# Optimization experiments

Hardware: AMD Instinct MI355X
Metric: run time of the kernel (lower is better)

The kernel has to match this reference:

```python
import jax, jax.numpy as jnp
import numpy as np

# Geometry constants (from init_kwargs)
LO = jnp.array([-51.2, -51.2, -3.0], dtype=jnp.float32)
HI = jnp.array([51.2, 51.2, 3.0], dtype=jnp.float32)
VS = jnp.array([0.2, 0.2, 6.0], dtype=jnp.float32)
NY, NX = 512, 512
BN_EPS = 1e-3  # mmdet3d BN1d default eps


def setup_inputs() -> dict:
    key = jax.random.key(0)
    ks = jax.random.split(key, 11)
    # points uniform inside point_cloud_range -> no points dropped by voxelizer
    points = jax.random.uniform(ks[0], (2, 120000, 3), dtype=jnp.float32) * (HI - LO) + LO
    C2, C = 32, 64
    w0 = jax.random.normal(ks[1], (8, C2), dtype=jnp.float32) / np.sqrt(8.0)
    g0 = jax.random.uniform(ks[2], (C2,), jnp.float32, 0.5, 1.5)
    b0 = jax.random.normal(ks[3], (C2,), jnp.float32) * 0.1
    m0 = jax.random.normal(ks[4], (C2,), jnp.float32) * 0.1
    v0 = jax.random.uniform(ks[5], (C2,), jnp.float32, 0.5, 1.5)
    w1 = jax.random.normal(ks[6], (C, C), dtype=jnp.float32) / np.sqrt(float(C))
    g1 = jax.random.uniform(ks[7], (C,), jnp.float32, 0.5, 1.5)
    b1 = jax.random.normal(ks[8], (C,), jnp.float32) * 0.1
    m1 = jax.random.normal(ks[9], (C,), jnp.float32) * 0.1
    v1 = jax.random.uniform(ks[10], (C,), jnp.float32, 0.5, 1.5)
    return dict(points=points, w0=w0, g0=g0, b0=b0, m0=m0, v0=v0,
                w1=w1, g1=g1, b1=b1, m1=m1, v1=v1)


def _bn(x, g, b, m, v):
    return (x - m) * jax.lax.rsqrt(v + BN_EPS) * g + b


def _embed_one(pts, w0, g0, b0, m0, v0, w1, g1, b1, m1, v1):
    # pts: [N, 3]. Dynamic voxelization: pillar index per point.
    xi = jnp.clip(jnp.floor((pts[:, 0] - LO[0]) / VS[0]).astype(jnp.int32), 0, NX - 1)
    yi = jnp.clip(jnp.floor((pts[:, 1] - LO[1]) / VS[1]).astype(jnp.int32), 0, NY - 1)
    vid = yi * NX + xi                       # flat pillar id, [N]
    nseg = NY * NX
    cnt = jax.ops.segment_sum(jnp.ones_like(pts[:, 0]), vid, nseg)  # [nseg]
    # cluster center offsets (mean xyz per pillar)
    mean = jax.ops.segment_sum(pts, vid, nseg) / jnp.maximum(cnt, 1.0)[:, None]
    f_cluster = pts - mean[vid]              # [N, 3]
    # pillar center offsets (x, y)
    cx = (xi.astype(pts.dtype) + 0.5) * VS[0] + LO[0]
    cy = (yi.astype(pts.dtype) + 0.5) * VS[1] + LO[1]
    f_center = jnp.stack([pts[:, 0] - cx, pts[:, 1] - cy], axis=-1)  # [N, 2]
    feats = jnp.concatenate([pts, f_cluster, f_center], axis=-1)     # [N, 8]
    # PFN layer 0: Linear(no bias) -> BN -> ReLU, then scatter-max + concat back
    h = jax.nn.relu(_bn(feats @ w0, g0, b0, m0, v0))                 # [N, 32]
    pooled0 = jax.ops.segment_max(h, vid, nseg)
    pooled0 = jnp.where(cnt[:, None] > 0, pooled0, 0.0)
    h = jnp.concatenate([h, pooled0[vid]], axis=-1)                  # [N, 64]
    # PFN layer 1 (last): per-point features, then scatter-max -> voxel feats
    h = jax.nn.relu(_bn(h @ w1, g1, b1, m1, v1))                     # [N, 64]
    vox = jax.ops.segment_max(h, vid, nseg)
    vox = jnp.where(cnt[:, None] > 0, vox, 0.0)                      # [nseg, 64]
    # PointPillarsScatter: dense BEV canvas [C, NY, NX]
    canvas = vox.reshape(NY, NX, -1).transpose(2, 0, 1)
    return canvas, h


def reference(points, w0, g0, b0, m0, v0, w1, g1, b1, m1, v1):
    canvases, point_feats = jax.vmap(
        lambda p: _embed_one(p, w0, g0, b0, m0, v0, w1, g1, b1, m1, v1)
    )(points)
    # canvases: [B, C, NY, NX] (torch.cat of per-sample pseudoimages over dim 0)
    return canvases, point_feats
```

## Files before the change

kernel.cpp:

```cpp
#include <hip/hip_runtime.h>

#define NPT   120000
#define NB    2
#define NSEG  262144
#define NXg   512
#define NSEGT (NB * NSEG)
#define NPTS  (NB * NPT)

typedef __attribute__((ext_vector_type(8))) short  bf16x8;
typedef __attribute__((ext_vector_type(4))) float  f32x4;

__device__ __forceinline__ unsigned short f2bf(float f) {
    unsigned u = __float_as_uint(f);
    return (unsigned short)((u + 0x7FFFu + ((u >> 16) & 1u)) >> 16);
}

__global__ __launch_bounds__(256) void k_init(unsigned int* __restrict__ cnt,
                                              const float* __restrict__ w1,
                                              const float* __restrict__ g1,
                                              const float* __restrict__ b1,
                                              const float* __restrict__ m1,
                                              const float* __restrict__ v1,
                                              unsigned short* __restrict__ wtbf,
                                              float* __restrict__ bias1f) {
    int t = threadIdx.x;
    if (blockIdx.x < 512) {
        int idx = blockIdx.x * 256 + t;
        ((uint4*)cnt)[idx] = make_uint4(0u, 0u, 0u, 0u);
        return;
    }
    #pragma unroll
    for (int i = 0; i < 16; ++i) {
        int idx = t + i * 256;
        int c = idx >> 6, k = idx & 63;
        float al = g1[c] * rsqrtf(v1[c] + 1e-3f);
        wtbf[idx] = f2bf(w1[k * 64 + c] * al);
    }
    if (t < 64) bias1f[t] = b1[t] - m1[t] * (g1[t] * rsqrtf(v1[t] + 1e-3f));
}

__global__ __launch_bounds__(256) void k_stats(const float* __restrict__ pts,
                                               unsigned int* __restrict__ cnt,
                                               unsigned int* __restrict__ rank) {
    int tid = blockIdx.x * 256 + threadIdx.x;
    if (tid >= NPTS) return;
    const float* p = pts + (size_t)tid * 3;
    float x = p[0], y = p[1];
    int xi = (int)floorf((x - (-51.2f)) / 0.2f);
    int yi = (int)floorf((y - (-51.2f)) / 0.2f);
    xi = min(max(xi, 0), 511);
    yi = min(max(yi, 0), 511);
    int b = (tid >= NPT) ? 1 : 0;
    int gvid = b * NSEG + (yi * NXg + xi);
    rank[tid] = atomicAdd(&cnt[gvid], 1u);
}

__global__ __launch_bounds__(256) void k_scan1(const unsigned int* __restrict__ cnt,
                                               unsigned int* __restrict__ offs,
                                               unsigned int* __restrict__ bsum) {
    __shared__ unsigned int s[256];
    int t = threadIdx.x;
    size_t base = (size_t)blockIdx.x * 1024 + t * 4;
    uint4 c4 = *(const uint4*)(cnt + base);
    unsigned int tsum = c4.x + c4.y + c4.z + c4.w;
    s[t] = tsum;
    __syncthreads();
    for (int o = 1; o < 256; o <<= 1) {
        unsigned int v = (t >= o) ? s[t - o] : 0u;
        __syncthreads();
        s[t] += v;
        __syncthreads();
    }
    unsigned int pre = s[t] - tsum;
    if (t == 255) bsum[blockIdx.x] = s[255];
    uint4 o4;
    o4.x = pre; o4.y = pre + c4.x; o4.z = o4.y + c4.y; o4.w = o4.z + c4.z;
    *(uint4*)(offs + base) = o4;
}

__global__ __launch_bounds__(256) void k_scan2(unsigned int* __restrict__ bsum) {
    __shared__ unsigned int s[256];
    int t = threadIdx.x;
    unsigned int a = bsum[2 * t], b = bsum[2 * t + 1];
    unsigned int ts = a + b;
    s[t] = ts;
    __syncthreads();
    for (int o = 1; o < 256; o <<= 1) {
        unsigned int v = (t >= o) ? s[t - o] : 0u;
        __syncthreads();
        s[t] += v;
        __syncthreads();
    }
    unsigned int pre = s[t] - ts;
    bsum[2 * t] = pre;
    bsum[2 * t + 1] = pre + a;
}

__global__ __launch_bounds__(256) void k_reorder(const float* __restrict__ pts,
                                                 const unsigned int* __restrict__ rank,
                                                 const unsigned int* __restrict__ offs,
                                                 const unsigned int* __restrict__ bsum,
                                                 float4* __restrict__ sxyz,
                                                 unsigned int* __restrict__ comb) {
    int tid = blockIdx.x * 256 + threadIdx.x;
    if (tid >= NPTS) return;
    const float* p = pts + (size_t)tid * 3;
    float x = p[0], y = p[1], z = p[2];
    int xi = (int)floorf((x - (-51.2f)) / 0.2f);
    int yi = (int)floorf((y - (-51.2f)) / 0.2f);
    xi = min(max(xi, 0), 511);
    yi = min(max(yi, 0), 511);
    int b = (tid >= NPT) ? 1 : 0;
    int gvid = b * NSEG + (yi * NXg + xi);
    unsigned pos = offs[gvid] + bsum[gvid >> 10] + rank[tid];
    sxyz[pos] = make_float4(x, y, z, __int_as_float(gvid));
    comb[pos] = ((unsigned)(gvid & 63) << 18) | (unsigned)tid;
}

__global__ __launch_bounds__(256) void k_pfn0(const float4* __restrict__ sxyz,
                                              const unsigned int* __restrict__ offs,
                                              const unsigned int* __restrict__ bsum,
                                              const unsigned int* __restrict__ cnt,
                                              const float* __restrict__ w0,
                                              const float* __restrict__ g0,
                                              const float* __restrict__ b0,
                                              const float* __restrict__ m0,
                                              const float* __restrict__ v0,
                                              unsigned short* __restrict__ xbf) {
    __shared__ float w0f[256];
    __shared__ float bias0[32];
    int t = threadIdx.x;
    {
        int c = t & 31;
        float al = g0[c] * rsqrtf(v0[c] + 1e-3f);
        w0f[t] = w0[t] * al;
        if (t < 32) bias0[t] = b0[t] - m0[t] * al;
    }
    __syncthreads();

    int pos = blockIdx.x * 256 + t;
    if (pos >= NPTS) return;

    float4 me = sxyz[pos];
    int gvid = __float_as_int(me.w);
    int vid = gvid & (NSEG - 1);
    int xi = vid & (NXg - 1), yi = vid >> 9;

    unsigned off = offs[gvid] + bsum[gvid >> 10];
    unsigned n   = cnt[gvid];
    float sx = 0.f, sy = 0.f, sz = 0.f;
    for (unsigned i = 0; i < n; ++i) {
        float4 q = sxyz[off + i];
        sx += q.x; sy += q.y; sz += q.z;
    }
    float inv = 1.0f / (float)n;
    float mx = sx * inv, my = sy * inv, mz = sz * inv;
    float cx = ((float)xi + 0.5f) * 0.2f + (-51.2f);
    float cy = ((float)yi + 0.5f) * 0.2f + (-51.2f);

    float own[32], pool[32];
    #pragma unroll
    for (int c = 0; c < 32; ++c) { pool[c] = 0.0f; own[c] = 0.0f; }
    for (unsigned i = 0; i < n; ++i) {
        float4 q = sxyz[off + i];
        float f[8] = {q.x, q.y, q.z, q.x - mx, q.y - my, q.z - mz,
                      q.x - cx, q.y - cy};
        bool self = (off + i == (unsigned)pos);
        #pragma unroll
        for (int c = 0; c < 32; ++c) {
            float acc = bias0[c];
            #pragma unroll
            for (int k = 0; k < 8; ++k) acc += f[k] * w0f[k * 32 + c];
            acc = fmaxf(acc, 0.0f);
            pool[c] = fmaxf(pool[c], acc);
            if (self) own[c] = acc;
        }
    }

    unsigned wv[16];
    uint4* dst = (uint4*)(xbf + (size_t)pos * 64);
    #pragma unroll
    for (int c2 = 0; c2 < 16; ++c2)
        wv[c2] = (unsigned)f2bf(own[2 * c2]) | ((unsigned)f2bf(own[2 * c2 + 1]) << 16);
    dst[0] = make_uint4(wv[0],  wv[1],  wv[2],  wv[3]);
    dst[1] = make_uint4(wv[4],  wv[5],  wv[6],  wv[7]);
    dst[2] = make_uint4(wv[8],  wv[9],  wv[10], wv[11]);
    dst[3] = make_uint4(wv[12], wv[13], wv[14], wv[15]);
    #pragma unroll
    for (int c2 = 0; c2 < 16; ++c2)
        wv[c2] = (unsigned)f2bf(pool[2 * c2]) | ((unsigned)f2bf(pool[2 * c2 + 1]) << 16);
    dst[4] = make_uint4(wv[0],  wv[1],  wv[2],  wv[3]);
    dst[5] = make_uint4(wv[4],  wv[5],  wv[6],  wv[7]);
    dst[6] = make_uint4(wv[8],  wv[9],  wv[10], wv[11]);
    dst[7] = make_uint4(wv[12], wv[13], wv[14], wv[15]);
}

__global__ __launch_bounds__(256) void k_pfn1(const unsigned short* __restrict__ xbf,
                                              const unsigned int* __restrict__ comb,
                                              const unsigned int* __restrict__ offs,
                                              const unsigned int* __restrict__ bsum,
                                              const unsigned short* __restrict__ wtbf,
                                              const float* __restrict__ bias1f,
                                              float* __restrict__ ptfeat,
                                              float* __restrict__ canvas) {
    __shared__ unsigned short xlds[64 * 64];
    __shared__ unsigned voxl[64][65];
    __shared__ unsigned combs[64];

    int t = threadIdx.x;
    int l = t & 63;
    int w = t >> 6;

    int batch = blockIdx.x >> 12;
    int vid0 = (blockIdx.x & 4095) << 6;
    int gvid0 = batch * NSEG + vid0;

    #pragma unroll
    for (int i = 0; i < 17; ++i) {
        int idx = t + i * 256;
        if (idx < 64 * 65) ((unsigned*)voxl)[idx] = 0u;
    }

    unsigned poslo = offs[gvid0] + bsum[gvid0 >> 10];
    int g2 = gvid0 + 64;
    unsigned poshi = (g2 < NSEGT) ? offs[g2] + bsum[g2 >> 10] : (unsigned)NPTS;

    bf16x8 bfr[4][2];
    float bia[4];
    #pragma unroll
    for (int n = 0; n < 4; ++n) {
        #pragma unroll
        for (int ks = 0; ks < 2; ++ks)
            bfr[n][ks] = *(const bf16x8*)(wtbf + ((n * 16 + (l & 15)) * 64 +
                                                  ks * 32 + (l >> 4) * 8));
        bia[n] = bias1f[n * 16 + (l & 15)];
    }
    __syncthreads();

    for (unsigned pc = poslo; pc < poshi; pc += 64) {
        unsigned m = min(64u, poshi - pc);

        for (int idx = t; idx < 512; idx += 256) {
            int pt = idx >> 3, seg = idx & 7;
            unsigned lin = (unsigned)(pt * 128 + seg * 16);
            unsigned swz = lin ^ ((unsigned)(pt & 7) << 4);
            bf16x8 val;
            #pragma unroll
            for (int e = 0; e < 8; ++e) val[e] = 0;
            if (pt < (int)m)
                val = *(const bf16x8*)(xbf + (size_t)(pc + pt) * 64 + seg * 8);
            *(bf16x8*)((char*)xlds + swz) = val;
        }
        for (int pt = t; pt < (int)m; pt += 256) combs[pt] = comb[pc + pt];
        __syncthreads();

        {
            int row = w * 16 + (l & 15);
            unsigned base = (unsigned)(row * 128 + ((l >> 4) << 4));
            unsigned sw = (unsigned)(row & 7) << 4;
            bf16x8 a0 = *(const bf16x8*)((char*)xlds + ((base + 0) ^ sw));
            bf16x8 a1 = *(const bf16x8*)((char*)xlds + ((base + 64) ^ sw));
            #pragma unroll
            for (int n = 0; n < 4; ++n) {
                f32x4 acc = {0.f, 0.f, 0.f, 0.f};
                acc = __builtin_amdgcn_mfma_f32_16x16x32_bf16(a0, bfr[n][0], acc, 0, 0, 0);
                acc = __builtin_amdgcn_mfma_f32_16x16x32_bf16(a1, bfr[n][1], acc, 0, 0, 0);
                int ch = n * 16 + (l & 15);
                #pragma unroll
                for (int r = 0; r < 4; ++r) {
                    int pidx = w * 16 + (l >> 4) * 4 + r;
                    if (pidx < (int)m) {
                        unsigned u = combs[pidx];
                        float v = fmaxf(acc[r] + bia[n], 0.0f);
                        ptfeat[(size_t)(u & 0x3FFFFu) * 64 + ch] = v;
                        atomicMax(&voxl[u >> 18][ch], __float_as_uint(v));
                    }
                }
            }
        }
        __syncthreads();
    }

    {
        float* cv = canvas + (size_t)batch * 64 * NSEG + vid0;
        #pragma unroll
        for (int i = 0; i < 16; ++i) {
            int c = i * 4 + w;
            cv[(size_t)c * NSEG + l] = __uint_as_float(voxl[l][c]);
        }
    }
}

extern "C" void kernel_launch(void* const* d_in, const int* in_sizes, int n_in,
                              void* d_out, int out_size, void* d_ws, size_t ws_size,
                              hipStream_t stream) {
    const float* pts = (const float*)d_in[0];
    const float* w0  = (const float*)d_in[1];
    const float* g0  = (const float*)d_in[2];
    const float* b0  = (const float*)d_in[3];
    const float* m0  = (const float*)d_in[4];
    const float* v0  = (const float*)d_in[5];
    const float* w1  = (const float*)d_in[6];
    const float* g1  = (const float*)d_in[7];
    const float* b1  = (const float*)d_in[8];
    const float* m1  = (const float*)d_in[9];
    const float* v1  = (const float*)d_in[10];
    float* out = (float*)d_out;
    float* ptfeat = out + (size_t)NB * 64 * NSEG;

    char* ws = (char*)d_ws;
    size_t off = 0;
    unsigned int* cnt   = (unsigned int*)(ws + off); off += (size_t)NSEGT * 4;
    unsigned int* offs  = (unsigned int*)(ws + off); off += (size_t)NSEGT * 4;
    unsigned int* rank  = (unsigned int*)(ws + off); off += (size_t)NPTS * 4;
    unsigned int* comb  = (unsigned int*)(ws + off); off += (size_t)NPTS * 4;
    float4* sxyz        = (float4*)(ws + off);       off += (size_t)NPTS * 16;
    unsigned short* xbf = (unsigned short*)(ws + off); off += (size_t)NPTS * 64 * 2;
    unsigned short* wtbf= (unsigned short*)(ws + off); off += 4096 * 2;
    float* bias1f       = (float*)(ws + off);        off += 64 * 4;
    unsigned int* bsum  = (unsigned int*)(ws + off); off += 512 * 4;

    int nblk = (NPTS + 255) / 256;
    k_init<<<513, 256, 0, stream>>>(cnt, w1, g1, b1, m1, v1, wtbf, bias1f);
    k_stats<<<nblk, 256, 0, stream>>>(pts, cnt, rank);
    k_scan1<<<NSEGT / 1024, 256, 0, stream>>>(cnt, offs, bsum);
    k_scan2<<<1, 256, 0, stream>>>(bsum);
    k_reorder<<<nblk, 256, 0, stream>>>(pts, rank, offs, bsum, sxyz, comb);
    k_pfn0<<<nblk, 256, 0, stream>>>(sxyz, offs, bsum, cnt,
                                     w0, g0, b0, m0, v0, xbf);
    k_pfn1<<<NB * 4096, 256, 0, stream>>>(xbf, comb, offs, bsum,
                                          wtbf, bias1f, ptfeat, out);
}
```

Measured before the change: 129.0 us.

## Fuse PFN layer 0 into PFN layer 1 kernel and merge scan passes

Computes the first PFN layer (cluster means, linear+BN+ReLU, per-pillar max) inside the MFMA-based second-layer kernel, writing bf16 features straight into LDS instead of round-tripping a global xbf buffer. Each point's 32 channels are split across 4 threads, and per-pillar offsets and counts are staged in LDS. The second scan launch is folded into the first using a last-block-done atomic ticket. This removes two kernel launches and about 30MB of global traffic, at the cost of redundant per-thread pillar loops, lower parallelism in the fused kernel, and higher LDS use.

```diff
diff --git a/kernel.cpp b/kernel.cpp
--- a/kernel.cpp
+++ b/kernel.cpp
@@ -22,7 +22,8 @@
                                               const float* __restrict__ m1,
                                               const float* __restrict__ v1,
                                               unsigned short* __restrict__ wtbf,
-                                              float* __restrict__ bias1f) {
+                                              float* __restrict__ bias1f,
+                                              unsigned int* __restrict__ tick) {
     int t = threadIdx.x;
     if (blockIdx.x < 512) {
         int idx = blockIdx.x * 256 + t;
@@ -37,6 +38,7 @@
         wtbf[idx] = f2bf(w1[k * 64 + c] * al);
     }
     if (t < 64) bias1f[t] = b1[t] - m1[t] * (g1[t] * rsqrtf(v1[t] + 1e-3f));
+    if (t == 0) *tick = 0u;
 }
 
 __global__ __launch_bounds__(256) void k_stats(const float* __restrict__ pts,
@@ -57,8 +59,10 @@
 
 __global__ __launch_bounds__(256) void k_scan1(const unsigned int* __restrict__ cnt,
                                                unsigned int* __restrict__ offs,
-                                               unsigned int* __restrict__ bsum) {
+                                               unsigned int* __restrict__ bsum,
+                                               unsigned int* __restrict__ tick) {
     __shared__ unsigned int s[256];
+    __shared__ int lastFlag;
     int t = threadIdx.x;
     size_t base = (size_t)blockIdx.x * 1024 + t * 4;
     uint4 c4 = *(const uint4*)(cnt + base);
@@ -76,14 +80,15 @@
     uint4 o4;
     o4.x = pre; o4.y = pre + c4.x; o4.z = o4.y + c4.y; o4.w = o4.z + c4.z;
     *(uint4*)(offs + base) = o4;
-}
-
-__global__ __launch_bounds__(256) void k_scan2(unsigned int* __restrict__ bsum) {
-    __shared__ unsigned int s[256];
-    int t = threadIdx.x;
-    unsigned int a = bsum[2 * t], b = bsum[2 * t + 1];
-    unsigned int ts = a + b;
-    s[t] = ts;
+
+    __threadfence();
+    if (t == 0) lastFlag = (atomicAdd(tick, 1u) == 511u);
+    __syncthreads();
+    if (!lastFlag) return;
+    unsigned a = __hip_atomic_load(&bsum[2 * t],     __ATOMIC_RELAXED, __HIP_MEMORY_SCOPE_AGENT);
+    unsigned b = __hip_atomic_load(&bsum[2 * t + 1], __ATOMIC_RELAXED, __HIP_MEMORY_SCOPE_AGENT);
+    unsigned ts2 = a + b;
+    s[t] = ts2;
     __syncthreads();
     for (int o = 1; o < 256; o <<= 1) {
         unsigned int v = (t >= o) ? s[t - o] : 0u;
@@ -91,9 +96,9 @@
         s[t] += v;
         __syncthreads();
     }
-    unsigned int pre = s[t] - ts;
-    bsum[2 * t] = pre;
-    bsum[2 * t + 1] = pre + a;
+    unsigned pre2 = s[t] - ts2;
+    bsum[2 * t] = pre2;
+    bsum[2 * t + 1] = pre2 + a;
 }
 
 __global__ __launch_bounds__(256) void k_reorder(const float* __restrict__ pts,
@@ -117,7 +122,8 @@
     comb[pos] = ((unsigned)(gvid & 63) << 18) | (unsigned)tid;
 }
 
-__global__ __launch_bounds__(256) void k_pfn0(const float4* __restrict__ sxyz,
+__global__ __launch_bounds__(256) void k_pfn1(const float4* __restrict__ sxyz,
+                                              const unsigned int* __restrict__ comb,
                                               const unsigned int* __restrict__ offs,
                                               const unsigned int* __restrict__ bsum,
                                               const unsigned int* __restrict__ cnt,
@@ -126,104 +132,49 @@
                                               const float* __restrict__ b0,
                                               const float* __restrict__ m0,
                                               const float* __restrict__ v0,
-                                              unsigned short* __restrict__ xbf) {
+                                              const unsigned short* __restrict__ wtbf,
+                                              const float* __restrict__ bias1f,
+                                              float* __restrict__ ptfeat,
+                                              float* __restrict__ canvas) {
     __shared__ float w0f[256];
     __shared__ float bias0[32];
+    __shared__ unsigned short xlds[64 * 64];
+    __shared__ unsigned voxl[64][65];
+    __shared__ unsigned combs[64];
+    __shared__ unsigned offl[64];
+    __shared__ unsigned cntl[64];
+
     int t = threadIdx.x;
+    int l = t & 63;
+    int w = t >> 6;
+
+    int batch = blockIdx.x >> 12;
+    int vid0 = (blockIdx.x & 4095) << 6;
+    int gvid0 = batch * NSEG + vid0;
+
     {
         int c = t & 31;
         float al = g0[c] * rsqrtf(v0[c] + 1e-3f);
         w0f[t] = w0[t] * al;
         if (t < 32) bias0[t] = b0[t] - m0[t] * al;
     }
-    __syncthreads();
-
-    int pos = blockIdx.x * 256 + t;
-    if (pos >= NPTS) return;
-
-    float4 me = sxyz[pos];
-    int gvid = __float_as_int(me.w);
-    int vid = gvid & (NSEG - 1);
-    int xi = vid & (NXg - 1), yi = vid >> 9;
-
-    unsigned off = offs[gvid] + bsum[gvid >> 10];
-    unsigned n   = cnt[gvid];
-    float sx = 0.f, sy = 0.f, sz = 0.f;
-    for (unsigned i = 0; i < n; ++i) {
-        float4 q = sxyz[off + i];
-        sx += q.x; sy += q.y; sz += q.z;
-    }
-    float inv = 1.0f / (float)n;
-    float mx = sx * inv, my = sy * inv, mz = sz * inv;
-    float cx = ((float)xi + 0.5f) * 0.2f + (-51.2f);
-    float cy = ((float)yi + 0.5f) * 0.2f + (-51.2f);
-
-    float own[32], pool[32];
-    #pragma unroll
-    for (int c = 0; c < 32; ++c) { pool[c] = 0.0f; own[c] = 0.0f; }
-    for (unsigned i = 0; i < n; ++i) {
-        float4 q = sxyz[off + i];
-        float f[8] = {q.x, q.y, q.z, q.x - mx, q.y - my, q.z - mz,
-                      q.x - cx, q.y - cy};
-        bool self = (off + i == (unsigned)pos);
-        #pragma unroll
-        for (int c = 0; c < 32; ++c) {
-            float acc = bias0[c];
-            #pragma unroll
-            for (int k = 0; k < 8; ++k) acc += f[k] * w0f[k * 32 + c];
-            acc = fmaxf(acc, 0.0f);
-            pool[c] = fmaxf(pool[c], acc);
-            if (self) own[c] = acc;
-        }
-    }
-
-    unsigned wv[16];
-    uint4* dst = (uint4*)(xbf + (size_t)pos * 64);
-    #pragma unroll
-    for (int c2 = 0; c2 < 16; ++c2)
-        wv[c2] = (unsigned)f2bf(own[2 * c2]) | ((unsigned)f2bf(own[2 * c2 + 1]) << 16);
-    dst[0] = make_uint4(wv[0],  wv[1],  wv[2],  wv[3]);
-    dst[1] = make_uint4(wv[4],  wv[5],  wv[6],  wv[7]);
-    dst[2] = make_uint4(wv[8],  wv[9],  wv[10], wv[11]);
-    dst[3] = make_uint4(wv[12], wv[13], wv[14], wv[15]);
-    #pragma unroll
-    for (int c2 = 0; c2 < 16; ++c2)
-        wv[c2] = (unsigned)f2bf(pool[2 * c2]) | ((unsigned)f2bf(pool[2 * c2 + 1]) << 16);
-    dst[4] = make_uint4(wv[0],  wv[1],  wv[2],  wv[3]);
-    dst[5] = make_uint4(wv[4],  wv[5],  wv[6],  wv[7]);
-    dst[6] = make_uint4(wv[8],  wv[9],  wv[10], wv[11]);
-    dst[7] = make_uint4(wv[12], wv[13], wv[14], wv[15]);
-}
-
-__global__ __launch_bounds__(256) void k_pfn1(const unsigned short* __restrict__ xbf,
-                                              const unsigned int* __restrict__ comb,
-                                              const unsigned int* __restrict__ offs,
-                                              const unsigned int* __restrict__ bsum,
-                                              const unsigned short* __restrict__ wtbf,
-                                              const float* __restrict__ bias1f,
-                                              float* __restrict__ ptfeat,
-                                              float* __restrict__ canvas) {
-    __shared__ unsigned short xlds[64 * 64];
-    __shared__ unsigned voxl[64][65];
-    __shared__ unsigned combs[64];
-
-    int t = threadIdx.x;
-    int l = t & 63;
-    int w = t >> 6;
-
-    int batch = blockIdx.x >> 12;
-    int vid0 = (blockIdx.x & 4095) << 6;
-    int gvid0 = batch * NSEG + vid0;
-
     #pragma unroll
     for (int i = 0; i < 17; ++i) {
         int idx = t + i * 256;
         if (idx < 64 * 65) ((unsigned*)voxl)[idx] = 0u;
     }
+    if (t < 64) {
+        int g = gvid0 + t;
+        offl[t] = offs[g] + bsum[g >> 10];
+        cntl[t] = cnt[g];
+    }
 
     unsigned poslo = offs[gvid0] + bsum[gvid0 >> 10];
-    int g2 = gvid0 + 64;
-    unsigned poshi = (g2 < NSEGT) ? offs[g2] + bsum[g2 >> 10] : (unsigned)NPTS;
+    unsigned poshi;
+    {
+        int g2 = gvid0 + 63;
+        poshi = offs[g2] + bsum[g2 >> 10] + cnt[g2];
+    }
 
     bf16x8 bfr[4][2];
     float bia[4];
@@ -240,18 +191,63 @@
     for (unsigned pc = poslo; pc < poshi; pc += 64) {
         unsigned m = min(64u, poshi - pc);
 
-        for (int idx = t; idx < 512; idx += 256) {
-            int pt = idx >> 3, seg = idx & 7;
-            unsigned lin = (unsigned)(pt * 128 + seg * 16);
-            unsigned swz = lin ^ ((unsigned)(pt & 7) << 4);
-            bf16x8 val;
-            #pragma unroll
-            for (int e = 0; e < 8; ++e) val[e] = 0;
-            if (pt < (int)m)
-                val = *(const bf16x8*)(xbf + (size_t)(pc + pt) * 64 + seg * 8);
-            *(bf16x8*)((char*)xlds + swz) = val;
+        {
+            int pt = t >> 2, j = t & 3;
+            unsigned sw = (unsigned)(pt & 7) << 4;
+            unsigned swz_own  = (unsigned)(pt * 128 + j * 16) ^ sw;
+            unsigned swz_pool = (unsigned)(pt * 128 + 64 + j * 16) ^ sw;
+            uint4 ow = make_uint4(0u, 0u, 0u, 0u);
+            uint4 pw = make_uint4(0u, 0u, 0u, 0u);
+            if (pt < (int)m) {
+                unsigned pos = pc + pt;
+                float4 me = sxyz[pos];
+                int gvid = __float_as_int(me.w);
+                int vloc = gvid & 63;
+                int vid = gvid & (NSEG - 1);
+                int xi = vid & (NXg - 1), yi = vid >> 9;
+                unsigned off = offl[vloc];
+                unsigned n = cntl[vloc];
+                float sx = 0.f, sy = 0.f, sz = 0.f;
+                for (unsigned i = 0; i < n; ++i) {
+                    float4 q = sxyz[off + i];
+                    sx += q.x; sy += q.y; sz += q.z;
+                }
+                float inv = 1.0f / (float)n;
+                float mx = sx * inv, my = sy * inv, mz = sz * inv;
+                float cx = ((float)xi + 0.5f) * 0.2f + (-51.2f);
+                float cy = ((float)yi + 0.5f) * 0.2f + (-51.2f);
+                float own[8], pool[8];
+                #pragma unroll
+                for (int c2 = 0; c2 < 8; ++c2) { own[c2] = 0.f; pool[c2] = 0.f; }
+                for (unsigned i = 0; i < n; ++i) {
+                    float4 q = sxyz[off + i];
+                    float f[8] = {q.x, q.y, q.z, q.x - mx, q.y - my, q.z - mz,
+                                  q.x - cx, q.y - cy};
+                    bool self = (off + i == pos);
+                    #pragma unroll
+                    for (int c2 = 0; c2 < 8; ++c2) {
+                        int c = j * 8 + c2;
+                        float acc = bias0[c];
+                        #pragma unroll
+                        for (int k = 0; k < 8; ++k) acc += f[k] * w0f[k * 32 + c];
+                        acc = fmaxf(acc, 0.0f);
+                        pool[c2] = fmaxf(pool[c2], acc);
+                        if (self) own[c2] = acc;
+                    }
+                }
+                ow.x = (unsigned)f2bf(own[0]) | ((unsigned)f2bf(own[1]) << 16);
+                ow.y = (unsigned)f2bf(own[2]) | ((unsigned)f2bf(own[3]) << 16);
+                ow.z = (unsigned)f2bf(own[4]) | ((unsigned)f2bf(own[5]) << 16);
+                ow.w = (unsigned)f2bf(own[6]) | ((unsigned)f2bf(own[7]) << 16);
+                pw.x = (unsigned)f2bf(pool[0]) | ((unsigned)f2bf(pool[1]) << 16);
+                pw.y = (unsigned)f2bf(pool[2]) | ((unsigned)f2bf(pool[3]) << 16);
+                pw.z = (unsigned)f2bf(pool[4]) | ((unsigned)f2bf(pool[5]) << 16);
+                pw.w = (unsigned)f2bf(pool[6]) | ((unsigned)f2bf(pool[7]) << 16);
+                if (j == 0) combs[pt] = comb[pos];
+            }
+            *(uint4*)((char*)xlds + swz_own) = ow;
+            *(uint4*)((char*)xlds + swz_pool) = pw;
         }
-        for (int pt = t; pt < (int)m; pt += 256) combs[pt] = comb[pc + pt];
         __syncthreads();
 
         {
@@ -315,19 +311,17 @@
     unsigned int* rank  = (unsigned int*)(ws + off); off += (size_t)NPTS * 4;
     unsigned int* comb  = (unsigned int*)(ws + off); off += (size_t)NPTS * 4;
     float4* sxyz        = (float4*)(ws + off);       off += (size_t)NPTS * 16;
-    unsigned short* xbf = (unsigned short*)(ws + off); off += (size_t)NPTS * 64 * 2;
     unsigned short* wtbf= (unsigned short*)(ws + off); off += 4096 * 2;
     float* bias1f       = (float*)(ws + off);        off += 64 * 4;
     unsigned int* bsum  = (unsigned int*)(ws + off); off += 512 * 4;
+    unsigned int* tick  = (unsigned int*)(ws + off); off += 4;
 
     int nblk = (NPTS + 255) / 256;
-    k_init<<<513, 256, 0, stream>>>(cnt, w1, g1, b1, m1, v1, wtbf, bias1f);
+    k_init<<<513, 256, 0, stream>>>(cnt, w1, g1, b1, m1, v1, wtbf, bias1f, tick);
     k_stats<<<nblk, 256, 0, stream>>>(pts, cnt, rank);
-    k_scan1<<<NSEGT / 1024, 256, 0, stream>>>(cnt, offs, bsum);
-    k_scan2<<<1, 256, 0, stream>>>(bsum);
+    k_scan1<<<NSEGT / 1024, 256, 0, stream>>>(cnt, offs, bsum, tick);
     k_reorder<<<nblk, 256, 0, stream>>>(pts, rank, offs, bsum, sxyz, comb);
-    k_pfn0<<<nblk, 256, 0, stream>>>(sxyz, offs, bsum, cnt,
-                                     w0, g0, b0, m0, v0, xbf);
-    k_pfn1<<<NB * 4096, 256, 0, stream>>>(xbf, comb, offs, bsum,
+    k_pfn1<<<NB * 4096, 256, 0, stream>>>(sxyz, comb, offs, bsum, cnt,
+                                          w0, g0, b0, m0, v0,
                                           wtbf, bias1f, ptfeat, out);
 }
```

Result: slower. 200.4 us (+55.3%).
